# Performance work log

Measured on AMD Instinct MI355X. Metric: run time of the kernel, lower is better.

The kernel has to match this reference:

```python
import jax, jax.numpy as jnp
import numpy as np

B, C, W, H = 8192, 512, 14, 4
D = C // H  # head dim = 128


def setup_inputs() -> dict:
    key = jax.random.key(0)
    ks = jax.random.split(key, 8)
    s = 1.0 / np.sqrt(C).astype(np.float32)
    return {
        "x": jax.random.normal(ks[0], (B, C, W), jnp.float32),
        "Wq": jax.random.normal(ks[1], (C, C), jnp.float32) * s,
        "bq": jax.random.normal(ks[2], (C,), jnp.float32) * 0.01,
        "Wk": jax.random.normal(ks[3], (C, C), jnp.float32) * s,
        "bk": jax.random.normal(ks[4], (C,), jnp.float32) * 0.01,
        "Wv": jax.random.normal(ks[5], (C, C), jnp.float32) * s,
        "bv": jax.random.normal(ks[6], (C,), jnp.float32) * 0.01,
        "rel_w": jax.random.normal(ks[7], (1, H, D, W), jnp.float32),
    }


def reference(x, Wq, bq, Wk, bk, Wv, bv, rel_w):
    # Conv1d(kernel_size=1) == channel-wise linear: out[b,o,w] = sum_c Wm[o,c]*x[b,c,w] + bm[o]
    def proj(Wm, bm):
        y = jnp.einsum('oc,bcw->bow', Wm, x) + bm[None, :, None]
        return y.reshape(B, H, D, W)

    q = proj(Wq, bq)  # [B,H,D,W]
    k = proj(Wk, bk)
    v = proj(Wv, bv)

    # content-content: q^T k over head dim -> [B,H,W,W]
    cc = jnp.einsum('bhdi,bhdj->bhij', q, k)
    # content-position: rel_w^T q -> [B,H,W,W] (rows = relative position, cols = query pos)
    cp = jnp.einsum('hdi,bhdj->bhij', rel_w[0], q)

    attn = jax.nn.softmax(cc + cp, axis=-1)  # softmax over last dim, as in the original

    # out = v @ attn^T : out[b,h,d,i] = sum_j v[b,h,d,j] * attn[b,h,i,j]
    out = jnp.einsum('bhdj,bhij->bhdi', v, attn)
    return out.reshape(B, C, W)
```

## Files before the change

kernel.cpp:

```cpp
#include <hip/hip_runtime.h>
#include <hip/hip_bf16.h>

typedef __bf16 bf16x8 __attribute__((ext_vector_type(8)));
typedef float f32x4 __attribute__((ext_vector_type(4)));
typedef int i32x4 __attribute__((ext_vector_type(4)));

typedef __attribute__((address_space(1))) const void GVoid;
typedef __attribute__((address_space(3))) void LVoid;

#define SX1 16.0f
#define SX1I 0.0625f
#define SX2 4000.0f
#define SW1 400.0f
#define SW1I 0.0025f
#define SW2 100000.0f
#define SR1 32.0f
#define SR1I 0.03125f
#define SR2 8000.0f
#define SC_QK 1.5625e-4f
#define SC_CP 1.953125e-3f
#define CORR 0.004f
#define QKS 4096.0f
#define QKSI 2.44140625e-4f
#define QKSI2 5.9604644775390625e-8f
#define CPS 256.0f
#define CPSI 3.90625e-3f

static __device__ __forceinline__ float b2f(unsigned short u) {
    union { float f; unsigned int i; } x; x.i = ((unsigned int)u) << 16; return x.f;
}
static __device__ __forceinline__ unsigned short f2b(float f) {
    union { float f; unsigned int u; } x; x.f = f;
    unsigned int r = x.u + 0x7FFFu + ((x.u >> 16) & 1u);
    return (unsigned short)(r >> 16);
}
static __device__ __forceinline__ int q8v(float v, float s) {
    int i = __float2int_rn(v * s);
    return (i > 127) ? 127 : (i < -127 ? -127 : i);
}
static __device__ __forceinline__ short f2s(float v, float s) {
    int i = __float2int_rn(v * s);
    i = (i > 32767) ? 32767 : (i < -32767 ? -32767 : i);
    return (short)i;
}
static __device__ __forceinline__ float s2f(unsigned int pair, int hi, float sc) {
    short s = hi ? (short)(pair >> 16) : (short)(pair & 0xffffu);
    return (float)s * sc;
}
static __device__ __forceinline__ void cvt8(uint4 r, float* o) {
    o[0] = (float)(short)(r.x & 0xffffu); o[1] = (float)(short)(r.x >> 16);
    o[2] = (float)(short)(r.y & 0xffffu); o[3] = (float)(short)(r.y >> 16);
    o[4] = (float)(short)(r.z & 0xffffu); o[5] = (float)(short)(r.z >> 16);
    o[6] = (float)(short)(r.w & 0xffffu); o[7] = (float)(short)(r.w >> 16);
}

__global__ __launch_bounds__(256) void k_prep(const float* __restrict__ Wq, const float* __restrict__ Wk,
                                              const float* __restrict__ Wv, const float* __restrict__ bq,
                                              const float* __restrict__ bk, const float* __restrict__ bv,
                                              const float* __restrict__ relw, char* __restrict__ Wi8,
                                              float* __restrict__ biasA) {
    int o = blockIdx.x;
    int tid = threadIdx.x;
    if (o < 1024) {
        const float* src = (o < 512) ? (Wq + (long)o * 512) : (Wk + (long)(o - 512) * 512);
        char* row = Wi8 + (long)o * 1024;
        for (int c = tid; c < 512; c += 256) {
            float w = src[c];
            int wh = q8v(w, SW1);
            float res = w - (float)wh * SW1I;
            int wl = q8v(res, SW2);
            row[c] = (char)wh;
            row[512 + c] = (char)wl;
        }
    } else if (o < 1536) {
        const float* src = Wv + (long)(o - 1024) * 512;
        char* row = Wi8 + (long)(1152 + (o - 1024)) * 1024;
        for (int c = tid; c < 512; c += 256) {
            float w = src[c];
            int wh = q8v(w, SW1);
            float res = w - (float)wh * SW1I;
            int wl = q8v(res, SW2);
            row[c] = (char)wh;
            row[512 + c] = (char)wl;
        }
    } else if (o < 1592) {
        int t = o - 1536, h = t / 14, i = t - h * 14;
        char* row = Wi8 + (long)(1024 + t) * 1024;
#pragma unroll
        for (int cc = 0; cc < 2; ++cc) {
            int c = tid + cc * 256;
            float acc = 0.f;
            for (int d = 0; d < 128; ++d)
                acc += relw[h * 1792 + d * 14 + i] * Wq[(long)(h * 128 + d) * 512 + c];
            int rh = q8v(acc, SR1);
            float res = acc - (float)rh * SR1I;
            int rl = q8v(res, SR2);
            row[c] = (char)rh;
            row[512 + c] = (char)rl;
        }
        if (tid == 0) {
            float acc = 0.f;
            for (int d = 0; d < 128; ++d) acc += relw[h * 1792 + d * 14 + i] * bq[h * 128 + d];
            biasA[1024 + t] = acc;
        }
    } else {
        for (int i = tid; i < 1664; i += 256) {
            if (i >= 1024 && i < 1080) continue;
            biasA[i] = (i < 512) ? bq[i] : (i < 1024) ? bk[i - 512] : (i < 1152) ? 0.f : bv[i - 1152];
        }
        int* z = (int*)(Wi8 + (long)1080 * 1024);
        for (int idx = tid; idx < 72 * 256; idx += 256) z[idx] = 0;
    }
}

__global__ __launch_bounds__(256) void k_transpose(const float* __restrict__ x,
                                                   char* __restrict__ Ai8, int b0) {
    __shared__ float xl[512 * 15];
    const float* xb = x + (long)(b0 + blockIdx.x) * 7168;
    const float4* xb4 = (const float4*)xb;
    int tid = threadIdx.x;
#pragma unroll
    for (int it = 0; it < 7; ++it) {
        int f = tid + it * 256;
        float4 v = xb4[f];
        float vals[4] = {v.x, v.y, v.z, v.w};
        int e = f * 4;
#pragma unroll
        for (int j = 0; j < 4; ++j) {
            int ee = e + j;
            int c = (ee * 9363) >> 17;
            int w = ee - c * 14;
            xl[c * 15 + w] = vals[j];
        }
    }
    __syncthreads();
    char* irow = Ai8 + (long)blockIdx.x * 14336;
#pragma unroll
    for (int it = 0; it < 7; ++it) {
        int p = tid + it * 256;
        int w = p >> 7, c0 = (p & 127) * 4;
        unsigned int hp = 0, lp = 0;
#pragma unroll
        for (int j = 0; j < 4; ++j) {
            float v = xl[(c0 + j) * 15 + w];
            int xh = q8v(v, SX1);
            float res = v - (float)xh * SX1I;
            int xlo = q8v(res, SX2);
            hp |= ((unsigned int)(xh & 255)) << (8 * j);
            lp |= ((unsigned int)(xlo & 255)) << (8 * j);
        }
        *(unsigned int*)(irow + (long)w * 1024 + c0) = hp;
        *(unsigned int*)(irow + (long)w * 1024 + 512 + c0) = lp;
    }
}

__global__ __launch_bounds__(256, 2) void k_fused(const char* __restrict__ Ai8,
                                                  const char* __restrict__ Wi8,
                                                  const float* __restrict__ biasA,
                                                  short* __restrict__ qkW,
                                                  unsigned short* __restrict__ vbW, int Mtiles,
                                                  const short* __restrict__ qkR,
                                                  const unsigned short* __restrict__ vbR,
                                                  float* __restrict__ out, int b0a) {
    __shared__ __align__(16) char LS[65536];
    int nG = Mtiles * 13;
    int tid = threadIdx.x;

    if ((int)blockIdx.x < nG) {
        int nwg = nG;
        int p = blockIdx.x;
        int xcd = p & 7, o8 = p >> 3;
        int q8_ = nwg >> 3, r8 = nwg & 7;
        int t = (xcd < r8 ? xcd * (q8_ + 1) : r8 * (q8_ + 1) + (xcd - r8) * q8_) + o8;
        int mt = t / 13, nt = t - mt * 13;
        long m0 = (long)mt * 128;
        int n0 = nt * 128;
        bool isv = (nt >= 9);
        int lane = tid & 63, wv = tid >> 6;
        int wr = wv >> 1, wc = wv & 1;

        i32x4 accM[4][4], accC[4][4];
#pragma unroll
        for (int i = 0; i < 4; ++i)
#pragma unroll
            for (int j = 0; j < 4; ++j) { accM[i][j] = (i32x4){0, 0, 0, 0}; accC[i][j] = (i32x4){0, 0, 0, 0}; }

#define STAGE(KT, BUF)                                                                           \
    {                                                                                            \
        int kof = (KT) * 64;                                                                     \
        _Pragma("unroll") for (int i = 0; i < 2; ++i) {                                          \
            int row = i * 64 + (tid >> 2);                                                       \
            int gu = (((tid & 3) + (row >> 1)) & 3) << 4;                                        \
            long ao = ((m0 + row) << 10) + kof + gu;                                             \
            long bo = ((long)(n0 + row) << 10) + kof + gu;                                       \
            int dof = (BUF) * 32768 + i * 4096 + tid * 16;                                       \
            __builtin_amdgcn_global_load_lds((GVoid*)(Ai8 + ao), (LVoid*)(LS + dof), 16, 0, 0);          \
            __builtin_amdgcn_global_load_lds((GVoid*)(Ai8 + ao + 512), (LVoid*)(LS + 8192 + dof), 16, 0, 0);  \
            __builtin_amdgcn_global_load_lds((GVoid*)(Wi8 + bo), (LVoid*)(LS + 16384 + dof), 16, 0, 0);       \
            __builtin_amdgcn_global_load_lds((GVoid*)(Wi8 + bo + 512), (LVoid*)(LS + 24576 + dof), 16, 0, 0); \
        }                                                                                        \
    }

        STAGE(0, 0);
        STAGE(1, 1);
        asm volatile("s_waitcnt vmcnt(8)" ::: "memory");
        __builtin_amdgcn_s_barrier();

        int cur = 0;
        for (int kt = 0; kt < 8; ++kt) {
            const char* Ah = LS + cur * 32768;
            const char* Al = Ah + 8192;
            const char* Bh = Ah + 16384;
            const char* Bl = Ah + 24576;
            int U = lane >> 4;
            i32x4 ah[4], al[4], bh[4], bl[4];
#pragma unroll
            for (int mf = 0; mf < 4; ++mf) {
                int row = wr * 64 + mf * 16 + (lane & 15);
                int off = row * 64 + (((U - (row >> 1)) & 3) << 4);
                ah[mf] = *(const i32x4*)(Ah + off);
                al[mf] = *(const i32x4*)(Al + off);
            }
#pragma unroll
            for (int nf = 0; nf < 4; ++nf) {
                int row = wc * 64 + nf * 16 + (lane & 15);
                int off = row * 64 + (((U - (row >> 1)) & 3) << 4);
                bh[nf] = *(const i32x4*)(Bh + off);
                bl[nf] = *(const i32x4*)(Bl + off);
            }
            asm volatile("s_waitcnt lgkmcnt(0)" ::: "memory");
            __builtin_amdgcn_sched_barrier(0);
            __builtin_amdgcn_s_barrier();
            if (kt + 2 < 8) STAGE(kt + 2, cur);

            __builtin_amdgcn_s_setprio(1);
#pragma unroll
            for (int mf = 0; mf < 4; ++mf)
#pragma unroll
                for (int nf = 0; nf < 4; ++nf)
                    accM[mf][nf] = __builtin_amdgcn_mfma_i32_16x16x64_i8(ah[mf], bh[nf], accM[mf][nf], 0, 0, 0);
#pragma unroll
            for (int mf = 0; mf < 4; ++mf)
#pragma unroll
                for (int nf = 0; nf < 4; ++nf) {
                    accC[mf][nf] = __builtin_amdgcn_mfma_i32_16x16x64_i8(al[mf], bh[nf], accC[mf][nf], 0, 0, 0);
                    accC[mf][nf] = __builtin_amdgcn_mfma_i32_16x16x64_i8(ah[mf], bl[nf], accC[mf][nf], 0, 0, 0);
                }
            __builtin_amdgcn_s_setprio(0);

            if (kt < 6) asm volatile("s_waitcnt vmcnt(8)" ::: "memory");
            else        asm volatile("s_waitcnt vmcnt(0)" ::: "memory");
            __builtin_amdgcn_sched_barrier(0);
            __builtin_amdgcn_s_barrier();
            cur ^= 1;
        }
#undef STAGE

        unsigned short* eb = (unsigned short*)LS;
#pragma unroll
        for (int nf = 0; nf < 4; ++nf) {
            int ncol = wc * 64 + nf * 16 + (lane & 15);
            int n = n0 + ncol;
            float scale = (n < 1024) ? SC_QK : (n < 1152 ? SC_CP : SC_QK);
            float qsc = (n < 1024) ? QKS : CPS;
            float bb = biasA[n];
#pragma unroll
            for (int mf = 0; mf < 4; ++mf) {
                int rl0 = wr * 64 + mf * 16 + ((lane >> 4) << 2);
#pragma unroll
                for (int r = 0; r < 4; ++r) {
                    float val = ((float)accM[mf][nf][r] + CORR * (float)accC[mf][nf][r]) * scale + bb;
                    unsigned short sv = isv ? f2b(val) : (unsigned short)f2s(val, qsc);
                    int row = rl0 + r;
                    eb[row * 128 + ((((ncol >> 3) ^ (row & 7)) << 3) | (ncol & 7))] = sv;
                }
            }
        }
        __syncthreads();
        {
            int row = tid >> 1, half = tid & 1;
            long rb = isv ? ((m0 + row) * 1024 + (long)(n0 - 1152) * 2)
                          : ((m0 + row) * 2304 + (long)n0 * 2);
            char* dst = (isv ? (char*)vbW : (char*)qkW) + rb + half * 128;
            const char* src = (const char*)eb + row * 256;
#pragma unroll
            for (int j = 0; j < 8; ++j) {
                int u = half * 8 + j;
                int up = u ^ (row & 7);
                *(uint4*)(dst + j * 16) = *(const uint4*)(src + up * 16);
            }
        }
    } else {
        unsigned short* qsI = (unsigned short*)LS;
        unsigned short* ksI = (unsigned short*)(LS + 14336);
        float* sl = (float*)(LS + 28672);
        int ab = (int)blockIdx.x - nG;
        long mb = (long)ab * 14;
        const uint4* qk16 = (const uint4*)qkR;
#pragma unroll
        for (int it = 0; it < 7; ++it) {
            int idx = tid + it * 256;
            int w = idx >> 7, c8 = idx & 127;
            uint4 raw = qk16[(mb + w) * 144 + c8];
            int u = c8 & 63;
            unsigned short* base = (c8 < 64) ? qsI : ksI;
            *(uint4*)&base[w * 512 + ((u ^ (w & 7)) << 3)] = raw;
        }
        __syncthreads();
        if (tid < 196) {
            int h = tid / 49, r = tid - h * 49;
            int i0 = (r / 7) * 2, j0 = (r - (r / 7) * 7) * 2;
            float a00 = 0.f, a01 = 0.f, a10 = 0.f, a11 = 0.f;
#pragma unroll
            for (int d8 = 0; d8 < 16; ++d8) {
                int uu = h * 16 + d8;
                uint4 ra = *(const uint4*)&qsI[i0 * 512 + ((uu ^ (i0 & 7)) << 3)];
                uint4 rb = *(const uint4*)&qsI[(i0 + 1) * 512 + ((uu ^ ((i0 + 1) & 7)) << 3)];
                uint4 rc = *(const uint4*)&ksI[j0 * 512 + ((uu ^ (j0 & 7)) << 3)];
                uint4 rd = *(const uint4*)&ksI[(j0 + 1) * 512 + ((uu ^ ((j0 + 1) & 7)) << 3)];
                float qa[8], qb[8], ka[8], kb[8];
                cvt8(ra, qa); cvt8(rb, qb); cvt8(rc, ka); cvt8(rd, kb);
#pragma unroll
                for (int e = 0; e < 8; ++e) {
                    a00 += qa[e] * ka[e];
                    a01 += qa[e] * kb[e];
                    a10 += qb[e] * ka[e];
                    a11 += qb[e] * kb[e];
                }
            }
            unsigned int cpa = *(const unsigned int*)&qkR[(mb + j0) * 1152 + 1024 + h * 14 + i0];
            unsigned int cpb = *(const unsigned int*)&qkR[(mb + j0 + 1) * 1152 + 1024 + h * 14 + i0];
            int base = (h * 14 + i0) * 16 + j0;
            sl[base]      = a00 * QKSI2 + s2f(cpa, 0, CPSI);
            sl[base + 16] = a10 * QKSI2 + s2f(cpa, 1, CPSI);
            sl[base + 1]  = a01 * QKSI2 + s2f(cpb, 0, CPSI);
            sl[base + 17] = a11 * QKSI2 + s2f(cpb, 1, CPSI);
        }
        __syncthreads();
        if (tid < 56) {
            float* row = &sl[tid * 16];
            float m = row[0];
#pragma unroll
            for (int j = 1; j < 14; ++j) m = fmaxf(m, row[j]);
            float ex[14]; float sum = 0.f;
#pragma unroll
            for (int j = 0; j < 14; ++j) { ex[j] = __expf(row[j] - m); sum += ex[j]; }
            float inv = 1.f / sum;
#pragma unroll
            for (int j = 0; j < 14; ++j) row[j] = ex[j] * inv;
        }
        __syncthreads();
#pragma unroll
        for (int cc = 0; cc < 2; ++cc) {
            int c = tid + cc * 256, h = c >> 7;
            float vr[14];
#pragma unroll
            for (int j = 0; j < 14; ++j) vr[j] = b2f(vbR[(mb + j) * 512 + c]);
            float* orow = out + (((long)(b0a + ab) * 512 + c) * 14);
            float ob[14];
#pragma unroll
            for (int i = 0; i < 14; ++i) {
                const float* ar = &sl[(h * 14 + i) * 16];
                float a = 0.f;
#pragma unroll
                for (int j = 0; j < 14; ++j) a += vr[j] * ar[j];
                ob[i] = a;
            }
#pragma unroll
            for (int t2 = 0; t2 < 7; ++t2)
                *(float2*)(orow + t2 * 2) = make_float2(ob[2 * t2], ob[2 * t2 + 1]);
        }
    }
}

extern "C" void kernel_launch(void* const* d_in, const int* in_sizes, int n_in,
                              void* d_out, int out_size, void* d_ws, size_t ws_size,
                              hipStream_t stream) {
    const float* x    = (const float*)d_in[0];
    const float* Wq   = (const float*)d_in[1];
    const float* bq   = (const float*)d_in[2];
    const float* Wk   = (const float*)d_in[3];
    const float* bk   = (const float*)d_in[4];
    const float* Wv   = (const float*)d_in[5];
    const float* bv   = (const float*)d_in[6];
    const float* relw = (const float*)d_in[7];
    float* out = (float*)d_out;
    char* ws = (char*)d_ws;

    char*  Wi8   = ws;
    float* biasA = (float*)(ws + 1703936);
    const long WS_DATA = 1712128;

    long avail = (long)ws_size - WS_DATA;
    long nbmax = avail / 107520;
    long NBc = (nbmax / 128) * 128;
    if (NBc > 2048) NBc = 2048;
    if (NBc < 128) NBc = 128;

    char*           Ai8  = ws + WS_DATA;
    short*          qkI0 = (short*)(Ai8 + NBc * 14336);
    short*          qkI1 = qkI0 + NBc * 16128;
    unsigned short* vb0  = (unsigned short*)(qkI1 + NBc * 16128);
    unsigned short* vb1  = vb0 + NBc * 7168;

    k_prep<<<1593, 256, 0, stream>>>(Wq, Wk, Wv, bq, bk, bv, relw, Wi8, biasA);

    int par = 0, prev_par = 0, prev_nb = 0, prev_b0 = 0;
    for (int b0 = 0; b0 < 8192; b0 += (int)NBc) {
        int nb = 8192 - b0; if (nb > NBc) nb = (int)NBc;
        k_transpose<<<nb, 256, 0, stream>>>(x, Ai8, b0);
        int Mtiles = (nb * 14) / 128;
        int nG = Mtiles * 13;
        short* qw = par ? qkI1 : qkI0;
        unsigned short* vw = par ? vb1 : vb0;
        const short* qr = prev_par ? qkI1 : qkI0;
        const unsigned short* vr = prev_par ? vb1 : vb0;
        k_fused<<<nG + prev_nb, 256, 0, stream>>>(Ai8, Wi8, biasA, qw, vw, Mtiles,
                                                  qr, vr, out, prev_b0);
        prev_nb = nb; prev_b0 = b0; prev_par = par; par ^= 1;
    }
    {
        const short* qr = prev_par ? qkI1 : qkI0;
        const unsigned short* vr = prev_par ? vb1 : vb0;
        k_fused<<<prev_nb, 256, 0, stream>>>(Ai8, Wi8, biasA, nullptr, nullptr, 0,
                                             qr, vr, out, prev_b0);
    }
}
```

Baseline: 635.0 us.

## Fuse next-chunk transpose into fused kernel and interleave attention blocks

Folds the per-chunk x transpose/quantize into the fused launch as extra blocks that prepare the next chunk's int8 activations into a double-buffered Ai8 workspace. The GEMM, attention and transpose work then overlap within one launch instead of running as separate serialized kernels. Attention blocks are also spread evenly among GEMM blocks by block-index interpolation rather than sitting at the end of the grid. The cost is a second Ai8 buffer, which reduces the maximum chunk size, plus added index arithmetic per block.

```diff
diff --git a/kernel.cpp b/kernel.cpp
--- a/kernel.cpp
+++ b/kernel.cpp
@@ -154,36 +154,43 @@
     }
 }
 
-__global__ __launch_bounds__(256, 2) void k_fused(const char* __restrict__ Ai8,
+__global__ __launch_bounds__(256, 2) void k_fused(const char* __restrict__ Ai8R,
+                                                  char* __restrict__ Ai8W,
+                                                  const float* __restrict__ x, int b0T, int nT,
                                                   const char* __restrict__ Wi8,
                                                   const float* __restrict__ biasA,
                                                   short* __restrict__ qkW,
                                                   unsigned short* __restrict__ vbW, int Mtiles,
                                                   const short* __restrict__ qkR,
                                                   const unsigned short* __restrict__ vbR,
-                                                  float* __restrict__ out, int b0a) {
+                                                  float* __restrict__ out, int b0a, int nA) {
     __shared__ __align__(16) char LS[65536];
     int nG = Mtiles * 13;
+    long totGA = (long)nG + nA;
     int tid = threadIdx.x;
-
-    if ((int)blockIdx.x < nG) {
-        int nwg = nG;
-        int p = blockIdx.x;
-        int xcd = p & 7, o8 = p >> 3;
-        int q8_ = nwg >> 3, r8 = nwg & 7;
-        int t = (xcd < r8 ? xcd * (q8_ + 1) : r8 * (q8_ + 1) + (xcd - r8) * q8_) + o8;
-        int mt = t / 13, nt = t - mt * 13;
-        long m0 = (long)mt * 128;
-        int n0 = nt * 128;
-        bool isv = (nt >= 9);
-        int lane = tid & 63, wv = tid >> 6;
-        int wr = wv >> 1, wc = wv & 1;
-
-        i32x4 accM[4][4], accC[4][4];
-#pragma unroll
-        for (int i = 0; i < 4; ++i)
-#pragma unroll
-            for (int j = 0; j < 4; ++j) { accM[i][j] = (i32x4){0, 0, 0, 0}; accC[i][j] = (i32x4){0, 0, 0, 0}; }
+    int bid = blockIdx.x;
+
+    if (bid < totGA) {
+        long ab = ((long)bid * nA) / totGA;
+        bool isAttn = (((long)(bid + 1) * nA) / totGA) > ab;
+        if (!isAttn) {
+            int nwg = nG;
+            int p = bid - (int)ab;
+            int xcd = p & 7, o8 = p >> 3;
+            int q8_ = nwg >> 3, r8 = nwg & 7;
+            int t = (xcd < r8 ? xcd * (q8_ + 1) : r8 * (q8_ + 1) + (xcd - r8) * q8_) + o8;
+            int mt = t / 13, nt = t - mt * 13;
+            long m0 = (long)mt * 128;
+            int n0 = nt * 128;
+            bool isv = (nt >= 9);
+            int lane = tid & 63, wv = tid >> 6;
+            int wr = wv >> 1, wc = wv & 1;
+
+            i32x4 accM[4][4], accC[4][4];
+#pragma unroll
+            for (int i = 0; i < 4; ++i)
+#pragma unroll
+                for (int j = 0; j < 4; ++j) { accM[i][j] = (i32x4){0, 0, 0, 0}; accC[i][j] = (i32x4){0, 0, 0, 0}; }
 
 #define STAGE(KT, BUF)                                                                           \
     {                                                                                            \
@@ -194,181 +201,219 @@
             long ao = ((m0 + row) << 10) + kof + gu;                                             \
             long bo = ((long)(n0 + row) << 10) + kof + gu;                                       \
             int dof = (BUF) * 32768 + i * 4096 + tid * 16;                                       \
-            __builtin_amdgcn_global_load_lds((GVoid*)(Ai8 + ao), (LVoid*)(LS + dof), 16, 0, 0);          \
-            __builtin_amdgcn_global_load_lds((GVoid*)(Ai8 + ao + 512), (LVoid*)(LS + 8192 + dof), 16, 0, 0);  \
+            __builtin_amdgcn_global_load_lds((GVoid*)(Ai8R + ao), (LVoid*)(LS + dof), 16, 0, 0);          \
+            __builtin_amdgcn_global_load_lds((GVoid*)(Ai8R + ao + 512), (LVoid*)(LS + 8192 + dof), 16, 0, 0);  \
             __builtin_amdgcn_global_load_lds((GVoid*)(Wi8 + bo), (LVoid*)(LS + 16384 + dof), 16, 0, 0);       \
             __builtin_amdgcn_global_load_lds((GVoid*)(Wi8 + bo + 512), (LVoid*)(LS + 24576 + dof), 16, 0, 0); \
         }                                                                                        \
     }
 
-        STAGE(0, 0);
-        STAGE(1, 1);
-        asm volatile("s_waitcnt vmcnt(8)" ::: "memory");
-        __builtin_amdgcn_s_barrier();
-
-        int cur = 0;
-        for (int kt = 0; kt < 8; ++kt) {
-            const char* Ah = LS + cur * 32768;
-            const char* Al = Ah + 8192;
-            const char* Bh = Ah + 16384;
-            const char* Bl = Ah + 24576;
-            int U = lane >> 4;
-            i32x4 ah[4], al[4], bh[4], bl[4];
-#pragma unroll
-            for (int mf = 0; mf < 4; ++mf) {
-                int row = wr * 64 + mf * 16 + (lane & 15);
-                int off = row * 64 + (((U - (row >> 1)) & 3) << 4);
-                ah[mf] = *(const i32x4*)(Ah + off);
-                al[mf] = *(const i32x4*)(Al + off);
-            }
+            STAGE(0, 0);
+            STAGE(1, 1);
+            asm volatile("s_waitcnt vmcnt(8)" ::: "memory");
+            __builtin_amdgcn_s_barrier();
+
+            int cur = 0;
+            for (int kt = 0; kt < 8; ++kt) {
+                const char* Ah = LS + cur * 32768;
+                const char* Al = Ah + 8192;
+                const char* Bh = Ah + 16384;
+                const char* Bl = Ah + 24576;
+                int U = lane >> 4;
+                i32x4 ah[4], al[4], bh[4], bl[4];
+#pragma unroll
+                for (int mf = 0; mf < 4; ++mf) {
+                    int row = wr * 64 + mf * 16 + (lane & 15);
+                    int off = row * 64 + (((U - (row >> 1)) & 3) << 4);
+                    ah[mf] = *(const i32x4*)(Ah + off);
+                    al[mf] = *(const i32x4*)(Al + off);
+                }
+#pragma unroll
+                for (int nf = 0; nf < 4; ++nf) {
+                    int row = wc * 64 + nf * 16 + (lane & 15);
+                    int off = row * 64 + (((U - (row >> 1)) & 3) << 4);
+                    bh[nf] = *(const i32x4*)(Bh + off);
+                    bl[nf] = *(const i32x4*)(Bl + off);
+                }
+                asm volatile("s_waitcnt lgkmcnt(0)" ::: "memory");
+                __builtin_amdgcn_sched_barrier(0);
+                __builtin_amdgcn_s_barrier();
+                if (kt + 2 < 8) STAGE(kt + 2, cur);
+
+                __builtin_amdgcn_s_setprio(1);
+#pragma unroll
+                for (int mf = 0; mf < 4; ++mf)
+#pragma unroll
+                    for (int nf = 0; nf < 4; ++nf)
+                        accM[mf][nf] = __builtin_amdgcn_mfma_i32_16x16x64_i8(ah[mf], bh[nf], accM[mf][nf], 0, 0, 0);
+#pragma unroll
+                for (int mf = 0; mf < 4; ++mf)
+#pragma unroll
+                    for (int nf = 0; nf < 4; ++nf) {
+                        accC[mf][nf] = __builtin_amdgcn_mfma_i32_16x16x64_i8(al[mf], bh[nf], accC[mf][nf], 0, 0, 0);
+                        accC[mf][nf] = __builtin_amdgcn_mfma_i32_16x16x64_i8(ah[mf], bl[nf], accC[mf][nf], 0, 0, 0);
+                    }
+                __builtin_amdgcn_s_setprio(0);
+
+                if (kt < 6) asm volatile("s_waitcnt vmcnt(8)" ::: "memory");
+                else        asm volatile("s_waitcnt vmcnt(0)" ::: "memory");
+                __builtin_amdgcn_sched_barrier(0);
+                __builtin_amdgcn_s_barrier();
+                cur ^= 1;
+            }
+#undef STAGE
+
+            unsigned short* eb = (unsigned short*)LS;
 #pragma unroll
             for (int nf = 0; nf < 4; ++nf) {
-                int row = wc * 64 + nf * 16 + (lane & 15);
-                int off = row * 64 + (((U - (row >> 1)) & 3) << 4);
-                bh[nf] = *(const i32x4*)(Bh + off);
-                bl[nf] = *(const i32x4*)(Bl + off);
-            }
-            asm volatile("s_waitcnt lgkmcnt(0)" ::: "memory");
-            __builtin_amdgcn_sched_barrier(0);
-            __builtin_amdgcn_s_barrier();
-            if (kt + 2 < 8) STAGE(kt + 2, cur);
-
-            __builtin_amdgcn_s_setprio(1);
-#pragma unroll
-            for (int mf = 0; mf < 4; ++mf)
-#pragma unroll
-                for (int nf = 0; nf < 4; ++nf)
-                    accM[mf][nf] = __builtin_amdgcn_mfma_i32_16x16x64_i8(ah[mf], bh[nf], accM[mf][nf], 0, 0, 0);
-#pragma unroll
-            for (int mf = 0; mf < 4; ++mf)
-#pragma unroll
-                for (int nf = 0; nf < 4; ++nf) {
-                    accC[mf][nf] = __builtin_amdgcn_mfma_i32_16x16x64_i8(al[mf], bh[nf], accC[mf][nf], 0, 0, 0);
-                    accC[mf][nf] = __builtin_amdgcn_mfma_i32_16x16x64_i8(ah[mf], bl[nf], accC[mf][nf], 0, 0, 0);
-                }
-            __builtin_amdgcn_s_setprio(0);
-
-            if (kt < 6) asm volatile("s_waitcnt vmcnt(8)" ::: "memory");
-            else        asm volatile("s_waitcnt vmcnt(0)" ::: "memory");
-            __builtin_amdgcn_sched_barrier(0);
-            __builtin_amdgcn_s_barrier();
-            cur ^= 1;
-        }
-#undef STAGE
-
-        unsigned short* eb = (unsigned short*)LS;
-#pragma unroll
-        for (int nf = 0; nf < 4; ++nf) {
-            int ncol = wc * 64 + nf * 16 + (lane & 15);
-            int n = n0 + ncol;
-            float scale = (n < 1024) ? SC_QK : (n < 1152 ? SC_CP : SC_QK);
-            float qsc = (n < 1024) ? QKS : CPS;
-            float bb = biasA[n];
-#pragma unroll
-            for (int mf = 0; mf < 4; ++mf) {
-                int rl0 = wr * 64 + mf * 16 + ((lane >> 4) << 2);
-#pragma unroll
-                for (int r = 0; r < 4; ++r) {
-                    float val = ((float)accM[mf][nf][r] + CORR * (float)accC[mf][nf][r]) * scale + bb;
-                    unsigned short sv = isv ? f2b(val) : (unsigned short)f2s(val, qsc);
-                    int row = rl0 + r;
-                    eb[row * 128 + ((((ncol >> 3) ^ (row & 7)) << 3) | (ncol & 7))] = sv;
-                }
+                int ncol = wc * 64 + nf * 16 + (lane & 15);
+                int n = n0 + ncol;
+                float scale = (n < 1024) ? SC_QK : (n < 1152 ? SC_CP : SC_QK);
+                float qsc = (n < 1024) ? QKS : CPS;
+                float bb = biasA[n];
+#pragma unroll
+                for (int mf = 0; mf < 4; ++mf) {
+                    int rl0 = wr * 64 + mf * 16 + ((lane >> 4) << 2);
+#pragma unroll
+                    for (int r = 0; r < 4; ++r) {
+                        float val = ((float)accM[mf][nf][r] + CORR * (float)accC[mf][nf][r]) * scale + bb;
+                        unsigned short sv = isv ? f2b(val) : (unsigned short)f2s(val, qsc);
+                        int row = rl0 + r;
+                        eb[row * 128 + ((((ncol >> 3) ^ (row & 7)) << 3) | (ncol & 7))] = sv;
+                    }
+                }
+            }
+            __syncthreads();
+            {
+                int row = tid >> 1, half = tid & 1;
+                long rb = isv ? ((m0 + row) * 1024 + (long)(n0 - 1152) * 2)
+                              : ((m0 + row) * 2304 + (long)n0 * 2);
+                char* dst = (isv ? (char*)vbW : (char*)qkW) + rb + half * 128;
+                const char* src = (const char*)eb + row * 256;
+#pragma unroll
+                for (int j = 0; j < 8; ++j) {
+                    int u = half * 8 + j;
+                    int up = u ^ (row & 7);
+                    *(uint4*)(dst + j * 16) = *(const uint4*)(src + up * 16);
+                }
+            }
+        } else {
+            unsigned short* qsI = (unsigned short*)LS;
+            unsigned short* ksI = (unsigned short*)(LS + 14336);
+            float* sl = (float*)(LS + 28672);
+            long mb = (long)ab * 14;
+            const uint4* qk16 = (const uint4*)qkR;
+#pragma unroll
+            for (int it = 0; it < 7; ++it) {
+                int idx = tid + it * 256;
+                int w = idx >> 7, c8 = idx & 127;
+                uint4 raw = qk16[(mb + w) * 144 + c8];
+                int u = c8 & 63;
+                unsigned short* base = (c8 < 64) ? qsI : ksI;
+                *(uint4*)&base[w * 512 + ((u ^ (w & 7)) << 3)] = raw;
+            }
+            __syncthreads();
+            if (tid < 196) {
+                int h = tid / 49, r = tid - h * 49;
+                int i0 = (r / 7) * 2, j0 = (r - (r / 7) * 7) * 2;
+                float a00 = 0.f, a01 = 0.f, a10 = 0.f, a11 = 0.f;
+#pragma unroll
+                for (int d8 = 0; d8 < 16; ++d8) {
+                    int uu = h * 16 + d8;
+                    uint4 ra = *(const uint4*)&qsI[i0 * 512 + ((uu ^ (i0 & 7)) << 3)];
+                    uint4 rb = *(const uint4*)&qsI[(i0 + 1) * 512 + ((uu ^ ((i0 + 1) & 7)) << 3)];
+                    uint4 rc = *(const uint4*)&ksI[j0 * 512 + ((uu ^ (j0 & 7)) << 3)];
+                    uint4 rd = *(const uint4*)&ksI[(j0 + 1) * 512 + ((uu ^ ((j0 + 1) & 7)) << 3)];
+                    float qa[8], qb[8], ka[8], kb[8];
+                    cvt8(ra, qa); cvt8(rb, qb); cvt8(rc, ka); cvt8(rd, kb);
+#pragma unroll
+                    for (int e = 0; e < 8; ++e) {
+                        a00 += qa[e] * ka[e];
+                        a01 += qa[e] * kb[e];
+                        a10 += qb[e] * ka[e];
+                        a11 += qb[e] * kb[e];
+                    }
+                }
+                unsigned int cpa = *(const unsigned int*)&qkR[(mb + j0) * 1152 + 1024 + h * 14 + i0];
+                unsigned int cpb = *(const unsigned int*)&qkR[(mb + j0 + 1) * 1152 + 1024 + h * 14 + i0];
+                int base = (h * 14 + i0) * 16 + j0;
+                sl[base]      = a00 * QKSI2 + s2f(cpa, 0, CPSI);
+                sl[base + 16] = a10 * QKSI2 + s2f(cpa, 1, CPSI);
+                sl[base + 1]  = a01 * QKSI2 + s2f(cpb, 0, CPSI);
+                sl[base + 17] = a11 * QKSI2 + s2f(cpb, 1, CPSI);
+            }
+            __syncthreads();
+            if (tid < 56) {
+                float* row = &sl[tid * 16];
+                float m = row[0];
+#pragma unroll
+                for (int j = 1; j < 14; ++j) m = fmaxf(m, row[j]);
+                float ex[14]; float sum = 0.f;
+#pragma unroll
+                for (int j = 0; j < 14; ++j) { ex[j] = __expf(row[j] - m); sum += ex[j]; }
+                float inv = 1.f / sum;
+#pragma unroll
+                for (int j = 0; j < 14; ++j) row[j] = ex[j] * inv;
+            }
+            __syncthreads();
+#pragma unroll
+            for (int cc = 0; cc < 2; ++cc) {
+                int c = tid + cc * 256, h = c >> 7;
+                float vr[14];
+#pragma unroll
+                for (int j = 0; j < 14; ++j) vr[j] = b2f(vbR[(mb + j) * 512 + c]);
+                float* orow = out + (((long)(b0a + ab) * 512 + c) * 14);
+                float ob[14];
+#pragma unroll
+                for (int i = 0; i < 14; ++i) {
+                    const float* ar = &sl[(h * 14 + i) * 16];
+                    float a = 0.f;
+#pragma unroll
+                    for (int j = 0; j < 14; ++j) a += vr[j] * ar[j];
+                    ob[i] = a;
+                }
+#pragma unroll
+                for (int t2 = 0; t2 < 7; ++t2)
+                    *(float2*)(orow + t2 * 2) = make_float2(ob[2 * t2], ob[2 * t2 + 1]);
+            }
+        }
+    } else {
+        float* xl = (float*)LS;
+        int tb = bid - (int)totGA;
+        const float* xb = x + (long)(b0T + tb) * 7168;
+        const float4* xb4 = (const float4*)xb;
+#pragma unroll
+        for (int it = 0; it < 7; ++it) {
+            int f = tid + it * 256;
+            float4 v = xb4[f];
+            float vals[4] = {v.x, v.y, v.z, v.w};
+            int e = f * 4;
+#pragma unroll
+            for (int j = 0; j < 4; ++j) {
+                int ee = e + j;
+                int c = (ee * 9363) >> 17;
+                int w = ee - c * 14;
+                xl[c * 15 + w] = vals[j];
             }
         }
         __syncthreads();
-        {
-            int row = tid >> 1, half = tid & 1;
-            long rb = isv ? ((m0 + row) * 1024 + (long)(n0 - 1152) * 2)
-                          : ((m0 + row) * 2304 + (long)n0 * 2);
-            char* dst = (isv ? (char*)vbW : (char*)qkW) + rb + half * 128;
-            const char* src = (const char*)eb + row * 256;
-#pragma unroll
-            for (int j = 0; j < 8; ++j) {
-                int u = half * 8 + j;
-                int up = u ^ (row & 7);
-                *(uint4*)(dst + j * 16) = *(const uint4*)(src + up * 16);
-            }
-        }
-    } else {
-        unsigned short* qsI = (unsigned short*)LS;
-        unsigned short* ksI = (unsigned short*)(LS + 14336);
-        float* sl = (float*)(LS + 28672);
-        int ab = (int)blockIdx.x - nG;
-        long mb = (long)ab * 14;
-        const uint4* qk16 = (const uint4*)qkR;
+        char* irow = Ai8W + (long)tb * 14336;
 #pragma unroll
         for (int it = 0; it < 7; ++it) {
-            int idx = tid + it * 256;
-            int w = idx >> 7, c8 = idx & 127;
-            uint4 raw = qk16[(mb + w) * 144 + c8];
-            int u = c8 & 63;
-            unsigned short* base = (c8 < 64) ? qsI : ksI;
-            *(uint4*)&base[w * 512 + ((u ^ (w & 7)) << 3)] = raw;
-        }
-        __syncthreads();
-        if (tid < 196) {
-            int h = tid / 49, r = tid - h * 49;
-            int i0 = (r / 7) * 2, j0 = (r - (r / 7) * 7) * 2;
-            float a00 = 0.f, a01 = 0.f, a10 = 0.f, a11 = 0.f;
-#pragma unroll
-            for (int d8 = 0; d8 < 16; ++d8) {
-                int uu = h * 16 + d8;
-                uint4 ra = *(const uint4*)&qsI[i0 * 512 + ((uu ^ (i0 & 7)) << 3)];
-                uint4 rb = *(const uint4*)&qsI[(i0 + 1) * 512 + ((uu ^ ((i0 + 1) & 7)) << 3)];
-                uint4 rc = *(const uint4*)&ksI[j0 * 512 + ((uu ^ (j0 & 7)) << 3)];
-                uint4 rd = *(const uint4*)&ksI[(j0 + 1) * 512 + ((uu ^ ((j0 + 1) & 7)) << 3)];
-                float qa[8], qb[8], ka[8], kb[8];
-                cvt8(ra, qa); cvt8(rb, qb); cvt8(rc, ka); cvt8(rd, kb);
-#pragma unroll
-                for (int e = 0; e < 8; ++e) {
-                    a00 += qa[e] * ka[e];
-                    a01 += qa[e] * kb[e];
-                    a10 += qb[e] * ka[e];
-                    a11 += qb[e] * kb[e];
-                }
-            }
-            unsigned int cpa = *(const unsigned int*)&qkR[(mb + j0) * 1152 + 1024 + h * 14 + i0];
-            unsigned int cpb = *(const unsigned int*)&qkR[(mb + j0 + 1) * 1152 + 1024 + h * 14 + i0];
-            int base = (h * 14 + i0) * 16 + j0;
-            sl[base]      = a00 * QKSI2 + s2f(cpa, 0, CPSI);
-            sl[base + 16] = a10 * QKSI2 + s2f(cpa, 1, CPSI);
-            sl[base + 1]  = a01 * QKSI2 + s2f(cpb, 0, CPSI);
-            sl[base + 17] = a11 * QKSI2 + s2f(cpb, 1, CPSI);
-        }
-        __syncthreads();
-        if (tid < 56) {
-            float* row = &sl[tid * 16];
-            float m = row[0];
-#pragma unroll
-            for (int j = 1; j < 14; ++j) m = fmaxf(m, row[j]);
-            float ex[14]; float sum = 0.f;
-#pragma unroll
-            for (int j = 0; j < 14; ++j) { ex[j] = __expf(row[j] - m); sum += ex[j]; }
-            float inv = 1.f / sum;
-#pragma unroll
-            for (int j = 0; j < 14; ++j) row[j] = ex[j] * inv;
-        }
-        __syncthreads();
-#pragma unroll
-        for (int cc = 0; cc < 2; ++cc) {
-            int c = tid + cc * 256, h = c >> 7;
-            float vr[14];
-#pragma unroll
-            for (int j = 0; j < 14; ++j) vr[j] = b2f(vbR[(mb + j) * 512 + c]);
-            float* orow = out + (((long)(b0a + ab) * 512 + c) * 14);
-            float ob[14];
-#pragma unroll
-            for (int i = 0; i < 14; ++i) {
-                const float* ar = &sl[(h * 14 + i) * 16];
-                float a = 0.f;
-#pragma unroll
-                for (int j = 0; j < 14; ++j) a += vr[j] * ar[j];
-                ob[i] = a;
-            }
-#pragma unroll
-            for (int t2 = 0; t2 < 7; ++t2)
-                *(float2*)(orow + t2 * 2) = make_float2(ob[2 * t2], ob[2 * t2 + 1]);
+            int p = tid + it * 256;
+            int w = p >> 7, c0 = (p & 127) * 4;
+            unsigned int hp = 0, lp = 0;
+#pragma unroll
+            for (int j = 0; j < 4; ++j) {
+                float v = xl[(c0 + j) * 15 + w];
+                int xh = q8v(v, SX1);
+                float res = v - (float)xh * SX1I;
+                int xlo = q8v(res, SX2);
+                hp |= ((unsigned int)(xh & 255)) << (8 * j);
+                lp |= ((unsigned int)(xlo & 255)) << (8 * j);
+            }
+            *(unsigned int*)(irow + (long)w * 1024 + c0) = hp;
+            *(unsigned int*)(irow + (long)w * 1024 + 512 + c0) = lp;
         }
     }
 }
@@ -392,37 +437,48 @@
     const long WS_DATA = 1712128;
 
     long avail = (long)ws_size - WS_DATA;
-    long nbmax = avail / 107520;
+    long nbmax = avail / 121856;
     long NBc = (nbmax / 128) * 128;
     if (NBc > 2048) NBc = 2048;
     if (NBc < 128) NBc = 128;
 
-    char*           Ai8  = ws + WS_DATA;
-    short*          qkI0 = (short*)(Ai8 + NBc * 14336);
-    short*          qkI1 = qkI0 + NBc * 16128;
-    unsigned short* vb0  = (unsigned short*)(qkI1 + NBc * 16128);
-    unsigned short* vb1  = vb0 + NBc * 7168;
+    char*           Ai8_0 = ws + WS_DATA;
+    char*           Ai8_1 = Ai8_0 + NBc * 14336;
+    short*          qkI0  = (short*)(Ai8_1 + NBc * 14336);
+    short*          qkI1  = qkI0 + NBc * 16128;
+    unsigned short* vb0   = (unsigned short*)(qkI1 + NBc * 16128);
+    unsigned short* vb1   = vb0 + NBc * 7168;
 
     k_prep<<<1593, 256, 0, stream>>>(Wq, Wk, Wv, bq, bk, bv, relw, Wi8, biasA);
+
+    int nb0 = (8192 < NBc) ? 8192 : (int)NBc;
+    k_transpose<<<nb0, 256, 0, stream>>>(x, Ai8_0, 0);
 
     int par = 0, prev_par = 0, prev_nb = 0, prev_b0 = 0;
     for (int b0 = 0; b0 < 8192; b0 += (int)NBc) {
         int nb = 8192 - b0; if (nb > NBc) nb = (int)NBc;
-        k_transpose<<<nb, 256, 0, stream>>>(x, Ai8, b0);
+        int next_b0 = b0 + nb;
+        int next_nb = 8192 - next_b0; if (next_nb > NBc) next_nb = (int)NBc; if (next_nb < 0) next_nb = 0;
         int Mtiles = (nb * 14) / 128;
         int nG = Mtiles * 13;
+
+        const char* aR = par ? Ai8_1 : Ai8_0;
+        char*       aW = par ? Ai8_0 : Ai8_1;
         short* qw = par ? qkI1 : qkI0;
         unsigned short* vw = par ? vb1 : vb0;
         const short* qr = prev_par ? qkI1 : qkI0;
         const unsigned short* vr = prev_par ? vb1 : vb0;
-        k_fused<<<nG + prev_nb, 256, 0, stream>>>(Ai8, Wi8, biasA, qw, vw, Mtiles,
-                                                  qr, vr, out, prev_b0);
+
+        k_fused<<<nG + prev_nb + next_nb, 256, 0, stream>>>(aR, aW, x, next_b0, next_nb,
+                                                            Wi8, biasA, qw, vw, Mtiles,
+                                                            qr, vr, out, prev_b0, prev_nb);
         prev_nb = nb; prev_b0 = b0; prev_par = par; par ^= 1;
     }
     {
         const short* qr = prev_par ? qkI1 : qkI0;
         const unsigned short* vr = prev_par ? vb1 : vb0;
-        k_fused<<<prev_nb, 256, 0, stream>>>(Ai8, Wi8, biasA, nullptr, nullptr, 0,
-                                             qr, vr, out, prev_b0);
-    }
-}
+        k_fused<<<prev_nb, 256, 0, stream>>>(nullptr, nullptr, x, 0, 0,
+                                             Wi8, biasA, nullptr, nullptr, 0,
+                                             qr, vr, out, prev_b0, prev_nb);
+    }
+}
```

After: 634.2 us. Within noise of the previous version (-0.1%).
